# Optimization experiments

Hardware: AMD Instinct MI355X
Metric: run time of the kernel (lower is better)

## Reference

```python
import jax, jax.numpy as jnp
import numpy as np

NEG_SLOPE = 0.2  # PyG GATConv default


def add_self_loops(edge_index, num_nodes):
    loops = jnp.arange(num_nodes, dtype=edge_index.dtype)
    return jnp.concatenate([edge_index, jnp.stack([loops, loops])], axis=1)


def gat_conv(x, edge_index, W, att_src, att_dst, bias, heads, out_ch, concat):
    # x: [N, F_in]; edge_index: [2, E] with row0=src(j), row1=dst(i)
    N = x.shape[0]
    xl = (x @ W).reshape(N, heads, out_ch)              # [N, H, C]
    src, dst = edge_index[0], edge_index[1]
    a_src = jnp.einsum('nhc,hc->nh', xl, att_src)        # [N, H]
    a_dst = jnp.einsum('nhc,hc->nh', xl, att_dst)        # [N, H]
    alpha = jax.nn.leaky_relu(a_src[src] + a_dst[dst], NEG_SLOPE)  # [E, H]
    # segment softmax over incoming edges of each dst node
    m = jax.ops.segment_max(alpha, dst, num_segments=N)  # [N, H]
    e = jnp.exp(alpha - m[dst])
    denom = jax.ops.segment_sum(e, dst, num_segments=N)
    coef = e / (denom[dst] + 1e-16)                      # [E, H]
    msg = xl[src] * coef[..., None]                      # [E, H, C]
    out = jax.ops.segment_sum(msg, dst, num_segments=N)  # [N, H, C]
    out = out.reshape(N, heads * out_ch) if concat else out.mean(axis=1)
    return out + bias


def setup_inputs() -> dict:
    key = jax.random.key(0)
    ks = jax.random.split(key, 12)
    N, E = 50000, 800000
    nfeat, nhid, nheads, nclass = 512, 8, 8, 16
    hid = nhid * nheads  # 64
    s1 = 1.0 / np.sqrt(nfeat)
    s2 = 1.0 / np.sqrt(hid)
    return {
        'x': jax.random.normal(ks[0], (N, nfeat), jnp.float32),
        'edge_index': jax.random.randint(ks[1], (2, E), 0, N, jnp.int64 if jax.config.jax_enable_x64 else jnp.int32),
        'W1': jax.random.uniform(ks[2], (nfeat, hid), jnp.float32, -s1, s1),
        'att_src1': jax.random.uniform(ks[3], (nheads, nhid), jnp.float32, -s2, s2),
        'att_dst1': jax.random.uniform(ks[4], (nheads, nhid), jnp.float32, -s2, s2),
        'bias1': jnp.zeros((hid,), jnp.float32),
        'W2': jax.random.uniform(ks[5], (hid, nclass), jnp.float32, -s2, s2),
        'att_src2': jax.random.uniform(ks[6], (1, nclass), jnp.float32, -0.25, 0.25),
        'att_dst2': jax.random.uniform(ks[7], (1, nclass), jnp.float32, -0.25, 0.25),
        'bias2': jnp.zeros((nclass,), jnp.float32),
    }


def reference(x, edge_index, W1, att_src1, att_dst1, bias1, W2, att_src2, att_dst2, bias2):
    N = x.shape[0]
    ei = add_self_loops(edge_index, N)
    # dropout layers are identity at inference
    h = gat_conv(x, ei, W1, att_src1, att_dst1, bias1, heads=8, out_ch=8, concat=True)
    o = gat_conv(h, ei, W2, att_src2, att_dst2, bias2, heads=1, out_ch=16, concat=True)
    o = jax.nn.elu(o)
    return jax.nn.log_softmax(o, axis=1)
```

## Files before the change

kernel.cpp:

```cpp
#include <hip/hip_runtime.h>
#include <math.h>

#define NEG_SLOPE 0.2f

typedef short short8 __attribute__((ext_vector_type(8)));
typedef float floatx4 __attribute__((ext_vector_type(4)));

static __device__ __forceinline__ float bf2f(unsigned short u) {
  return __uint_as_float(((unsigned int)u) << 16);
}
static __device__ __forceinline__ unsigned short f2bf(float f) {
  unsigned int u = __float_as_uint(f);
  u = (u + 0x7fffu + ((u >> 16) & 1u)) >> 16;
  return (unsigned short)u;
}
static __device__ __forceinline__ unsigned int pack2(float a, float b) {
  return (unsigned int)f2bf(a) | ((unsigned int)f2bf(b) << 16);
}

__global__ void init_misc(const float* __restrict__ W1, unsigned short* __restrict__ W1t,
                          int* __restrict__ deg, int N) {
  int b = blockIdx.x;
  if (b < 128) {
    int i = b * 256 + threadIdx.x;
    int k = i >> 6, c = i & 63;
    W1t[c * 512 + k] = f2bf(W1[i]);
  } else {
    int n = (b - 128) * 256 + threadIdx.x;
    if (n < N) deg[n] = 1;
  }
}

__global__ __launch_bounds__(256) void gemm1_hist(const float* __restrict__ A,
                                                  const unsigned short* __restrict__ W1t,
                                                  const float* __restrict__ att_src,
                                                  const float* __restrict__ att_dst,
                                                  unsigned short* __restrict__ xlb,
                                                  float* __restrict__ a_src,
                                                  float* __restrict__ a_dst, int M,
                                                  const int* __restrict__ ei,
                                                  int* __restrict__ deg, int E,
                                                  int ipc, int G1) {
  if ((int)blockIdx.x >= G1) {
    int b = blockIdx.x - G1;
    int slice = b & 7;
    int chunk = b >> 3;
    int lo = (int)(((long long)slice * M) >> 3);
    int hi = (int)(((long long)(slice + 1) * M) >> 3);
    int beg = chunk * ipc;
    int end = min(beg + ipc, E);
    for (int i = beg + threadIdx.x; i < end; i += 256) {
      int d = ei[E + i];
      if (d >= lo && d < hi) atomicAdd(&deg[d], 1);
    }
    return;
  }
  int tid = threadIdx.x;
  int w = tid >> 6, lane = tid & 63;
  int q = lane >> 4, cl = lane & 15;
  int row0 = blockIdx.x << 6;
  int ar = row0 + w * 16 + cl;
  int arc = ar < M ? ar : 0;
  const float* Ap = A + (size_t)arc * 512 + q * 8;
  const unsigned short* Bp = W1t + cl * 512 + q * 8;
  floatx4 acc[4] = {};

#pragma unroll
  for (int ks = 0; ks < 16; ++ks) {
    int k0 = ks * 32;
    float4 fa = *(const float4*)(Ap + k0);
    float4 fb = *(const float4*)(Ap + k0 + 4);
    union { uint4 u; short8 s; } cva;
    cva.u.x = pack2(fa.x, fa.y);
    cva.u.y = pack2(fa.z, fa.w);
    cva.u.z = pack2(fb.x, fb.y);
    cva.u.w = pack2(fb.z, fb.w);
#pragma unroll
    for (int t = 0; t < 4; ++t) {
      short8 bf = *(const short8*)(Bp + t * 16 * 512 + k0);
      acc[t] = __builtin_amdgcn_mfma_f32_16x16x32_bf16(cva.s, bf, acc[t], 0, 0, 0);
    }
  }

  float asv[4], adv[4];
#pragma unroll
  for (int t = 0; t < 4; ++t) {
    asv[t] = att_src[t * 16 + cl];
    adv[t] = att_dst[t * 16 + cl];
  }
#pragma unroll
  for (int reg = 0; reg < 4; ++reg) {
    int r = row0 + w * 16 + q * 4 + reg;
    bool ok = r < M;
#pragma unroll
    for (int t = 0; t < 4; ++t) {
      float v = acc[t][reg];
      if (ok) xlb[(size_t)r * 64 + t * 16 + cl] = f2bf(v);
      float ps = v * asv[t];
      float pd = v * adv[t];
      ps += __shfl_xor(ps, 1); pd += __shfl_xor(pd, 1);
      ps += __shfl_xor(ps, 2); pd += __shfl_xor(pd, 2);
      ps += __shfl_xor(ps, 4); pd += __shfl_xor(pd, 4);
      if (ok && (cl & 7) == 0) {
        int h = t * 2 + (cl >> 3);
        a_src[r * 8 + h] = ps;
        a_dst[r * 8 + h] = pd;
      }
    }
  }
}

__global__ __launch_bounds__(1024) void scan_single(const int* __restrict__ deg,
                                                    int* __restrict__ rowptr,
                                                    int* __restrict__ cursor, int N) {
  __shared__ int wsum[16];
  int tid = threadIdx.x;
  int lane = tid & 63, wv = tid >> 6;
  int carry = 0;
  for (int base = 0; base < N; base += 8192) {
    int i0 = base + tid * 8;
    int d[8];
    if (i0 + 8 <= N) {
      int4 a = *(const int4*)(deg + i0);
      int4 b = *(const int4*)(deg + i0 + 4);
      d[0] = a.x; d[1] = a.y; d[2] = a.z; d[3] = a.w;
      d[4] = b.x; d[5] = b.y; d[6] = b.z; d[7] = b.w;
    } else {
#pragma unroll
      for (int k = 0; k < 8; ++k) d[k] = (i0 + k < N) ? deg[i0 + k] : 0;
    }
    int e[8];
    e[0] = d[0];
#pragma unroll
    for (int k = 1; k < 8; ++k) e[k] = e[k - 1] + d[k];
    int tot = e[7];
    int v = tot;
#pragma unroll
    for (int off = 1; off < 64; off <<= 1) {
      int t = __shfl_up(v, off, 64);
      if (lane >= off) v += t;
    }
    if (lane == 63) wsum[wv] = v;
    __syncthreads();
    int woff = carry;
    for (int w = 0; w < wv; ++w) woff += wsum[w];
    int excl = woff + v - tot;
    int r[8];
    r[0] = excl;
#pragma unroll
    for (int k = 1; k < 8; ++k) r[k] = excl + e[k - 1];
    if (i0 + 8 <= N) {
      *(int4*)(rowptr + i0)     = make_int4(r[0], r[1], r[2], r[3]);
      *(int4*)(rowptr + i0 + 4) = make_int4(r[4], r[5], r[6], r[7]);
      *(int4*)(cursor + i0)     = make_int4(r[0], r[1], r[2], r[3]);
      *(int4*)(cursor + i0 + 4) = make_int4(r[4], r[5], r[6], r[7]);
    } else {
#pragma unroll
      for (int k = 0; k < 8; ++k)
        if (i0 + k < N) { rowptr[i0 + k] = r[k]; cursor[i0 + k] = r[k]; }
    }
    int bt = 0;
#pragma unroll
    for (int w = 0; w < 16; ++w) bt += wsum[w];
    carry += bt;
    __syncthreads();
  }
  if (tid == 0) rowptr[N] = carry;
}

__global__ __launch_bounds__(256) void scatter_sliced(const int* __restrict__ ei,
                                                      int* __restrict__ cursor,
                                                      int* __restrict__ srcs,
                                                      int E, int N, int ipc) {
  int slice = blockIdx.x & 7;
  int chunk = blockIdx.x >> 3;
  int lo = (int)(((long long)slice * N) >> 3);
  int hi = (int)(((long long)(slice + 1) * N) >> 3);
  int total = E + N;
  int beg = chunk * ipc;
  int end = min(beg + ipc, total);
  for (int i = beg + threadIdx.x; i < end; i += 256) {
    int d = (i < E) ? ei[E + i] : (i - E);
    if (d >= lo && d < hi) {
      int s = (i < E) ? ei[i] : d;
      int pos = atomicAdd(&cursor[d], 1);
      srcs[pos] = s;
    }
  }
}

__global__ __launch_bounds__(256) void agg1_fused(const int* __restrict__ rowptr,
                                                  const int* __restrict__ srcs,
                                                  const float* __restrict__ a_src,
                                                  const float* __restrict__ a_dst,
                                                  const unsigned short* __restrict__ xlb,
                                                  const float* __restrict__ bias1,
                                                  const float* __restrict__ W2,
                                                  const float* __restrict__ att_src2,
                                                  const float* __restrict__ att_dst2,
                                                  float* __restrict__ xl2,
                                                  float* __restrict__ a_src2,
                                                  float* __restrict__ a_dst2, int N) {
  __shared__ float W2s[64 * 16];
  __shared__ float hsm[4][64];
  int tid = threadIdx.x;
  W2s[tid]       = W2[tid];
  W2s[tid + 256] = W2[tid + 256];
  W2s[tid + 512] = W2[tid + 512];
  W2s[tid + 768] = W2[tid + 768];
  __syncthreads();

  int wv = tid >> 6, lane = tid & 63;
  int node = (blockIdx.x << 2) + wv;
  if (node >= N) return;
  int half = lane >> 5;
  int j = lane & 31;
  int h = j >> 2;
  int beg = rowptr[node], end = rowptr[node + 1];
  float ad = a_dst[node * 8 + h];
  float den = 0.f, acc0 = 0.f, acc1 = 0.f;

  int p = beg + half;
  bool v0 = p < end, v1 = p + 2 < end, v2 = p + 4 < end, v3 = p + 6 < end;
  int s0 = srcs[v0 ? p : beg];
  int s1 = srcs[v1 ? p + 2 : beg];
  int s2 = srcs[v2 ? p + 4 : beg];
  int s3 = srcs[v3 ? p + 6 : beg];
  while (v0) {
    int np = p + 8;
    bool u0 = np < end, u1 = np + 2 < end, u2 = np + 4 < end, u3 = np + 6 < end;
    int t0 = srcs[u0 ? np : beg];
    int t1 = srcs[u1 ? np + 2 : beg];
    int t2 = srcs[u2 ? np + 4 : beg];
    int t3 = srcs[u3 ? np + 6 : beg];
    float a0 = a_src[s0 * 8 + h] + ad;
    float a1 = a_src[s1 * 8 + h] + ad;
    float a2 = a_src[s2 * 8 + h] + ad;
    float a3 = a_src[s3 * 8 + h] + ad;
    ushort2 x0 = *(const ushort2*)(xlb + (size_t)s0 * 64 + 2 * j);
    ushort2 x1 = *(const ushort2*)(xlb + (size_t)s1 * 64 + 2 * j);
    ushort2 x2 = *(const ushort2*)(xlb + (size_t)s2 * 64 + 2 * j);
    ushort2 x3 = *(const ushort2*)(xlb + (size_t)s3 * 64 + 2 * j);
    a0 = a0 >= 0.f ? a0 : NEG_SLOPE * a0;
    a1 = a1 >= 0.f ? a1 : NEG_SLOPE * a1;
    a2 = a2 >= 0.f ? a2 : NEG_SLOPE * a2;
    a3 = a3 >= 0.f ? a3 : NEG_SLOPE * a3;
    float w0 = v0 ? __expf(a0) : 0.f;
    float w1 = v1 ? __expf(a1) : 0.f;
    float w2 = v2 ? __expf(a2) : 0.f;
    float w3 = v3 ? __expf(a3) : 0.f;
    den += (w0 + w1) + (w2 + w3);
    acc0 += w0 * bf2f(x0.x) + w1 * bf2f(x1.x) + w2 * bf2f(x2.x) + w3 * bf2f(x3.x);
    acc1 += w0 * bf2f(x0.y) + w1 * bf2f(x1.y) + w2 * bf2f(x2.y) + w3 * bf2f(x3.y);
    p = np;
    s0 = t0; s1 = t1; s2 = t2; s3 = t3;
    v0 = u0; v1 = u1; v2 = u2; v3 = u3;
  }
  den  += __shfl_xor(den, 32);
  acc0 += __shfl_xor(acc0, 32);
  acc1 += __shfl_xor(acc1, 32);
  float inv = 1.f / (den + 1e-16f);
  float2 bv = *(const float2*)(bias1 + 2 * j);
  float h0 = acc0 * inv + bv.x;
  float h1 = acc1 * inv + bv.y;
  if (half == 0) {
    hsm[wv][2 * j]     = h0;
    hsm[wv][2 * j + 1] = h1;
  }
  if (lane < 16) {
    float sum = 0.f;
#pragma unroll
    for (int k = 0; k < 64; ++k) sum += hsm[wv][k] * W2s[k * 16 + lane];
    xl2[(size_t)node * 16 + lane] = sum;
    float ps = sum * att_src2[lane];
    float pd = sum * att_dst2[lane];
#pragma unroll
    for (int w = 8; w >= 1; w >>= 1) {
      ps += __shfl_xor(ps, w, 16);
      pd += __shfl_xor(pd, w, 16);
    }
    if (lane == 0) { a_src2[node] = ps; a_dst2[node] = pd; }
  }
}

__global__ __launch_bounds__(256) void agg2_fin(const int* __restrict__ rowptr,
                                                const int* __restrict__ srcs,
                                                const float* __restrict__ a_src2,
                                                const float* __restrict__ a_dst2,
                                                const float* __restrict__ xl2,
                                                const float* __restrict__ bias2,
                                                float* __restrict__ out, int N) {
  int t = blockIdx.x * blockDim.x + threadIdx.x;
  int node = t >> 4;
  int c = t & 15;
  if (node >= N) return;
  int beg = rowptr[node], end = rowptr[node + 1];
  float ad = a_dst2[node];
  float den = 0.f, acc = 0.f;
  int p = beg;
  bool v0 = true, v1 = p + 1 < end, v2 = p + 2 < end, v3 = p + 3 < end;
  int s0 = srcs[p];
  int s1 = srcs[v1 ? p + 1 : beg];
  int s2 = srcs[v2 ? p + 2 : beg];
  int s3 = srcs[v3 ? p + 3 : beg];
  while (v0) {
    int np = p + 4;
    bool u0 = np < end, u1 = np + 1 < end, u2 = np + 2 < end, u3 = np + 3 < end;
    int t0 = srcs[u0 ? np : beg];
    int t1 = srcs[u1 ? np + 1 : beg];
    int t2 = srcs[u2 ? np + 2 : beg];
    int t3 = srcs[u3 ? np + 3 : beg];
    float a0 = a_src2[s0] + ad, a1 = a_src2[s1] + ad;
    float a2 = a_src2[s2] + ad, a3 = a_src2[s3] + ad;
    float x0 = xl2[(size_t)s0 * 16 + c], x1 = xl2[(size_t)s1 * 16 + c];
    float x2 = xl2[(size_t)s2 * 16 + c], x3 = xl2[(size_t)s3 * 16 + c];
    a0 = a0 >= 0.f ? a0 : NEG_SLOPE * a0;
    a1 = a1 >= 0.f ? a1 : NEG_SLOPE * a1;
    a2 = a2 >= 0.f ? a2 : NEG_SLOPE * a2;
    a3 = a3 >= 0.f ? a3 : NEG_SLOPE * a3;
    float w0 = v0 ? __expf(a0) : 0.f;
    float w1 = v1 ? __expf(a1) : 0.f;
    float w2 = v2 ? __expf(a2) : 0.f;
    float w3 = v3 ? __expf(a3) : 0.f;
    den += (w0 + w1) + (w2 + w3);
    acc += w0 * x0 + w1 * x1 + w2 * x2 + w3 * x3;
    p = np;
    s0 = t0; s1 = t1; s2 = t2; s3 = t3;
    v0 = u0; v1 = u1; v2 = u2; v3 = u3;
  }
  float o = acc / (den + 1e-16f) + bias2[c];
  o = o > 0.f ? o : expm1f(o);
  float mx = o;
#pragma unroll
  for (int w = 8; w >= 1; w >>= 1) mx = fmaxf(mx, __shfl_xor(mx, w, 16));
  float e = __expf(o - mx);
  float ssum = e;
#pragma unroll
  for (int w = 8; w >= 1; w >>= 1) ssum += __shfl_xor(ssum, w, 16);
  out[(size_t)node * 16 + c] = o - mx - logf(ssum);
}

static inline size_t rnd16(size_t x) { return (x + 15) & ~(size_t)15; }

extern "C" void kernel_launch(void* const* d_in, const int* in_sizes, int n_in,
                              void* d_out, int out_size, void* d_ws, size_t ws_size,
                              hipStream_t stream) {
  const float* x        = (const float*)d_in[0];
  const int*   ei       = (const int*)d_in[1];
  const float* W1       = (const float*)d_in[2];
  const float* att_src1 = (const float*)d_in[3];
  const float* att_dst1 = (const float*)d_in[4];
  const float* bias1    = (const float*)d_in[5];
  const float* W2       = (const float*)d_in[6];
  const float* att_src2 = (const float*)d_in[7];
  const float* att_dst2 = (const float*)d_in[8];
  const float* bias2    = (const float*)d_in[9];
  float* out = (float*)d_out;

  int N = in_sizes[0] / 512;
  int E = in_sizes[1] / 2;

  char* ws = (char*)d_ws;
  unsigned short* xlb = (unsigned short*)ws;  ws += rnd16((size_t)N * 64 * 2);
  unsigned short* W1t = (unsigned short*)ws;  ws += rnd16((size_t)512 * 64 * 2);
  float* a_src1 = (float*)ws;                 ws += rnd16((size_t)N * 8 * 4);
  float* a_dst1 = (float*)ws;                 ws += rnd16((size_t)N * 8 * 4);
  float* xl2    = (float*)ws;                 ws += rnd16((size_t)N * 16 * 4);
  float* a_src2 = (float*)ws;                 ws += rnd16((size_t)N * 4);
  float* a_dst2 = (float*)ws;                 ws += rnd16((size_t)N * 4);
  int* deg      = (int*)ws;                   ws += rnd16((size_t)N * 4);
  int* rowptr   = (int*)ws;                   ws += rnd16((size_t)(N + 1) * 4);
  int* cursor   = (int*)ws;                   ws += rnd16((size_t)N * 4);
  int* srcs     = (int*)ws;                   ws += rnd16((size_t)(E + N) * 4);

  const int NCHUNK = 256;
  int G1 = (N + 63) / 64;
  int ipc_h = (E + NCHUNK - 1) / NCHUNK;
  int ipc_s = (E + N + NCHUNK - 1) / NCHUNK;

  init_misc<<<128 + (N + 255) / 256, 256, 0, stream>>>(W1, W1t, deg, N);
  gemm1_hist<<<G1 + NCHUNK * 8, 256, 0, stream>>>(x, W1t, att_src1, att_dst1,
                                                  xlb, a_src1, a_dst1, N,
                                                  ei, deg, E, ipc_h, G1);
  scan_single<<<1, 1024, 0, stream>>>(deg, rowptr, cursor, N);
  scatter_sliced<<<NCHUNK * 8, 256, 0, stream>>>(ei, cursor, srcs, E, N, ipc_s);
  agg1_fused<<<(N + 3) / 4, 256, 0, stream>>>(rowptr, srcs, a_src1, a_dst1, xlb,
                                              bias1, W2, att_src2, att_dst2,
                                              xl2, a_src2, a_dst2, N);
  agg2_fin<<<((size_t)N * 16 + 255) / 256, 256, 0, stream>>>(rowptr, srcs, a_src2, a_dst2,
                                                             xl2, bias2, out, N);
}
```

Baseline: 320.4 us.

## Split GEMM1 K-dimension across waves with shared-memory reduction

Each block now handles 16 rows instead of 64, and its four waves each compute a quarter of the K=512 reduction, after which the partial sums are combined through a shared-memory buffer. This quadruples the number of GEMM blocks and shortens each wave's serial MFMA chain, aiming to expose more parallelism and memory-level concurrency for the x load. The cost is a 16 KB LDS allocation, which now also applies to the histogram blocks and can lower their occupancy, plus an extra __syncthreads and reduction step.

```diff
diff --git a/kernel.cpp b/kernel.cpp
--- a/kernel.cpp
+++ b/kernel.cpp
@@ -41,6 +41,7 @@
                                                   const int* __restrict__ ei,
                                                   int* __restrict__ deg, int E,
                                                   int ipc, int G1) {
+  __shared__ float red[4][16][64];
   if ((int)blockIdx.x >= G1) {
     int b = blockIdx.x - G1;
     int slice = b & 7;
@@ -56,17 +57,17 @@
     return;
   }
   int tid = threadIdx.x;
-  int w = tid >> 6, lane = tid & 63;
+  int wv = tid >> 6, lane = tid & 63;
   int q = lane >> 4, cl = lane & 15;
-  int row0 = blockIdx.x << 6;
-  int ar = row0 + w * 16 + cl;
+  int row0 = blockIdx.x << 4;
+  int ar = row0 + cl;
   int arc = ar < M ? ar : 0;
-  const float* Ap = A + (size_t)arc * 512 + q * 8;
-  const unsigned short* Bp = W1t + cl * 512 + q * 8;
+  const float* Ap = A + (size_t)arc * 512 + wv * 128 + q * 8;
+  const unsigned short* Bp = W1t + cl * 512 + wv * 128 + q * 8;
   floatx4 acc[4] = {};
 
 #pragma unroll
-  for (int ks = 0; ks < 16; ++ks) {
+  for (int ks = 0; ks < 4; ++ks) {
     int k0 = ks * 32;
     float4 fa = *(const float4*)(Ap + k0);
     float4 fb = *(const float4*)(Ap + k0 + 4);
@@ -82,30 +83,37 @@
     }
   }
 
+#pragma unroll
+  for (int t = 0; t < 4; ++t)
+#pragma unroll
+    for (int reg = 0; reg < 4; ++reg)
+      red[wv][q * 4 + reg][t * 16 + cl] = acc[t][reg];
+  __syncthreads();
+
+  int row = tid >> 4, c0 = tid & 15;
+  int r = row0 + row;
+  bool ok = r < M;
   float asv[4], adv[4];
 #pragma unroll
   for (int t = 0; t < 4; ++t) {
-    asv[t] = att_src[t * 16 + cl];
-    adv[t] = att_dst[t * 16 + cl];
-  }
-#pragma unroll
-  for (int reg = 0; reg < 4; ++reg) {
-    int r = row0 + w * 16 + q * 4 + reg;
-    bool ok = r < M;
-#pragma unroll
-    for (int t = 0; t < 4; ++t) {
-      float v = acc[t][reg];
-      if (ok) xlb[(size_t)r * 64 + t * 16 + cl] = f2bf(v);
-      float ps = v * asv[t];
-      float pd = v * adv[t];
-      ps += __shfl_xor(ps, 1); pd += __shfl_xor(pd, 1);
-      ps += __shfl_xor(ps, 2); pd += __shfl_xor(pd, 2);
-      ps += __shfl_xor(ps, 4); pd += __shfl_xor(pd, 4);
-      if (ok && (cl & 7) == 0) {
-        int h = t * 2 + (cl >> 3);
-        a_src[r * 8 + h] = ps;
-        a_dst[r * 8 + h] = pd;
-      }
+    asv[t] = att_src[t * 16 + c0];
+    adv[t] = att_dst[t * 16 + c0];
+  }
+#pragma unroll
+  for (int t = 0; t < 4; ++t) {
+    int col = t * 16 + c0;
+    float v = (red[0][row][col] + red[1][row][col]) +
+              (red[2][row][col] + red[3][row][col]);
+    if (ok) xlb[(size_t)r * 64 + col] = f2bf(v);
+    float ps = v * asv[t];
+    float pd = v * adv[t];
+    ps += __shfl_xor(ps, 1); pd += __shfl_xor(pd, 1);
+    ps += __shfl_xor(ps, 2); pd += __shfl_xor(pd, 2);
+    ps += __shfl_xor(ps, 4); pd += __shfl_xor(pd, 4);
+    if (ok && (c0 & 7) == 0) {
+      int h = t * 2 + (c0 >> 3);
+      a_src[r * 8 + h] = ps;
+      a_dst[r * 8 + h] = pd;
     }
   }
 }
@@ -374,7 +382,7 @@
   int* srcs     = (int*)ws;                   ws += rnd16((size_t)(E + N) * 4);
 
   const int NCHUNK = 256;
-  int G1 = (N + 63) / 64;
+  int G1 = (N + 15) / 16;
   int ipc_h = (E + NCHUNK - 1) / NCHUNK;
   int ipc_s = (E + N + NCHUNK - 1) / NCHUNK;
 
```

Result: slower. 327.2 us (+2.1%).
